# Performance work log

Measured on AMD Instinct MI355X. Metric: run time of the kernel, lower is better.

## Reference

```python
import jax, jax.numpy as jnp
import numpy as np

N_NODES = 100000
N_EDGES = 1000000
D_FEAT = 64


def setup_inputs() -> dict:
    key = jax.random.key(0)
    k1, k2 = jax.random.split(key)
    x = jax.random.normal(k1, (N_NODES, D_FEAT), dtype=jnp.float32)
    es = jax.random.randint(k2, (2, N_EDGES), 0, N_NODES, dtype=jnp.int32)
    return {"x": x, "es": es}


def reference(x, es):
    # message (option='o2i'): col, row = es ; x_i = x[row], x_o = x[col]
    col, row = es[0], es[1]
    x_i = x[row]                              # [E, D]
    x_o = x[col]                              # [E, D]
    msg = jnp.concatenate([x_i, x_o], axis=-1)  # [E, 2D]
    n = x.shape[0]
    # aggregate: scatter-mean over idx=col
    summed = jax.ops.segment_sum(msg, col, num_segments=n)          # [N, 2D]
    ones = jnp.ones((es.shape[1],), dtype=x.dtype)
    count = jax.ops.segment_sum(ones, col, num_segments=n)          # [N]
    count = jnp.maximum(count, 1.0)[:, None]  # clamp(min=1), broadcast
    return summed / count
```

## Files before the change

### kernel.cpp

```cpp
#include <hip/hip_runtime.h>

#define D 64
#define SH 9
#define CPB 512
#define CH 4096
#define MAXNB 256


__global__ __launch_bounds__(256) void count_kernel(
    const int* __restrict__ es, int* __restrict__ cmat,
    int NB, int NBLK, int E) {
  __shared__ int hist[MAXNB];
  int t = threadIdx.x;
  hist[t] = 0;
  __syncthreads();
  int base_e = blockIdx.x * CH;
#pragma unroll
  for (int j = 0; j < 16; j++) {
    int e = base_e + t + j * 256;
    if (e < E) atomicAdd(&hist[es[e] >> SH], 1);
  }
  __syncthreads();
  if (t < NB) cmat[t * NBLK + blockIdx.x] = hist[t];
}

__global__ __launch_bounds__(256) void scanP1(
    int* __restrict__ cmat, int* __restrict__ bsums, int M) {
  __shared__ int lds[256];
  int t = threadIdx.x;
  int base = blockIdx.x * 1024 + t * 4;
  int v[4], s = 0;
#pragma unroll
  for (int i = 0; i < 4; i++) {
    v[i] = (base + i < M) ? cmat[base + i] : 0;
    s += v[i];
  }
  lds[t] = s;
  __syncthreads();
  for (int off = 1; off < 256; off <<= 1) {
    int val = (t >= off) ? lds[t - off] : 0;
    __syncthreads();
    lds[t] += val;
    __syncthreads();
  }
  int run = lds[t] - s;
#pragma unroll
  for (int i = 0; i < 4; i++) {
    if (base + i < M) cmat[base + i] = run;
    run += v[i];
  }
  if (t == 255) bsums[blockIdx.x] = lds[255];
}

__global__ __launch_bounds__(256) void scanP2(
    int* __restrict__ bsums, int* __restrict__ bbase,
    int* __restrict__ offsets, int nb, int NB, int N, int E) {
  __shared__ int lds[256];
  int t = threadIdx.x;
  int v = (t < nb) ? bsums[t] : 0;
  lds[t] = v;
  __syncthreads();
  for (int off = 1; off < 256; off <<= 1) {
    int val = (t >= off) ? lds[t - off] : 0;
    __syncthreads();
    lds[t] += val;
    __syncthreads();
  }
  if (t < nb) bsums[t] = lds[t] - v;
  if (t == 0) { bbase[NB] = E; offsets[N] = E; }
}

__global__ __launch_bounds__(256) void scanP3(
    int* __restrict__ cmat, const int* __restrict__ bsums,
    int* __restrict__ bbase, int M, int NBLK) {
  int t = threadIdx.x;
  int add = bsums[blockIdx.x];
  int base = blockIdx.x * 1024 + t * 4;
#pragma unroll
  for (int i = 0; i < 4; i++) {
    int idx = base + i;
    if (idx < M) {
      int v = cmat[idx] + add;
      cmat[idx] = v;
      if (idx % NBLK == 0) bbase[idx / NBLK] = v;
    }
  }
}

__global__ __launch_bounds__(256) void scatter_kernel(
    const int* __restrict__ es, const int* __restrict__ cmat,
    int* __restrict__ packed, int NB, int NBLK, int E) {
  __shared__ int hist[MAXNB];
  __shared__ int lstart[MAXNB];
  __shared__ int gbase[MAXNB];
  __shared__ int cursor[MAXNB];
  __shared__ int sctmp[256];
  __shared__ int staged[CH];
  __shared__ int bidl[CH];
  int t = threadIdx.x;
  hist[t] = 0;
  __syncthreads();
  int base_e = blockIdx.x * CH;
  int c[16], r[16];
#pragma unroll
  for (int j = 0; j < 16; j++) {
    int e = base_e + t + j * 256;
    if (e < E) {
      c[j] = es[e];
      r[j] = es[E + e];
      atomicAdd(&hist[c[j] >> SH], 1);
    } else {
      c[j] = -1;
    }
  }
  __syncthreads();
  int v = hist[t];
  sctmp[t] = v;
  __syncthreads();
  for (int off = 1; off < 256; off <<= 1) {
    int val = (t >= off) ? sctmp[t - off] : 0;
    __syncthreads();
    sctmp[t] += val;
    __syncthreads();
  }
  int excl = sctmp[t] - v;
  lstart[t] = excl;
  cursor[t] = excl;
  if (t < NB) gbase[t] = cmat[t * NBLK + blockIdx.x];
  __syncthreads();
#pragma unroll
  for (int j = 0; j < 16; j++) {
    if (c[j] >= 0) {
      int b = c[j] >> SH;
      int rank = atomicAdd(&cursor[b], 1);
      staged[rank] = (r[j] << SH) | (c[j] & (CPB - 1));
      bidl[rank] = b;
    }
  }
  __syncthreads();
  int nloc = min(CH, E - base_e);
  for (int i = t; i < nloc; i += 256) {
    int b = bidl[i];
    packed[gbase[b] + (i - lstart[b])] = staged[i];
  }
}

__global__ __launch_bounds__(256) void sort_cols(
    const int* __restrict__ packed, const int* __restrict__ bbase,
    int* __restrict__ offsets, int* __restrict__ sorted_rows, int N) {
  __shared__ int cnt[CPB];
  __shared__ int sctmp[256];
  __shared__ int cur[CPB];
  int b = blockIdx.x;
  int t = threadIdx.x;
  int s = bbase[b], e = bbase[b + 1];
  cnt[t] = 0;
  cnt[t + 256] = 0;
  __syncthreads();
  for (int i = s + t; i < e; i += 256) atomicAdd(&cnt[packed[i] & (CPB - 1)], 1);
  __syncthreads();
  int c0 = cnt[2 * t], c1 = cnt[2 * t + 1];
  int pair = c0 + c1;
  sctmp[t] = pair;
  __syncthreads();
  for (int off = 1; off < 256; off <<= 1) {
    int val = (t >= off) ? sctmp[t - off] : 0;
    __syncthreads();
    sctmp[t] += val;
    __syncthreads();
  }
  int excl = sctmp[t] - pair;
  cur[2 * t] = excl;
  cur[2 * t + 1] = excl + c0;
  int gc0 = (b << SH) + 2 * t;
  if (gc0 < N) offsets[gc0] = s + excl;
  if (gc0 + 1 < N) offsets[gc0 + 1] = s + excl + c0;
  __syncthreads();
  for (int i = s + t; i < e; i += 256) {
    int p = packed[i];
    int cc = p & (CPB - 1);
    int rank = atomicAdd(&cur[cc], 1);
    sorted_rows[s + rank] = p >> SH;
  }
}

__global__ __launch_bounds__(256) void node_reduce(
    const float4* __restrict__ x4, const int* __restrict__ sorted_rows,
    const int* __restrict__ offsets, float* __restrict__ out, int N) {
  int gid = blockIdx.x * 256 + threadIdx.x;
  int node = gid >> 6;
  if (node >= N) return;
  int lane = threadIdx.x & 63;
  int eg = lane >> 4;
  int d16 = lane & 15;
  int start = offsets[node];
  int cnt = offsets[node + 1] - start;
  float4 a0 = make_float4(0.f, 0.f, 0.f, 0.f);
  float4 a1 = make_float4(0.f, 0.f, 0.f, 0.f);
  float4 a2 = make_float4(0.f, 0.f, 0.f, 0.f);
  float4 a3 = make_float4(0.f, 0.f, 0.f, 0.f);
  for (int base = 0; base < cnt; base += 16) {
    int k0 = base + eg;
    int k1 = base + 4 + eg;
    int k2 = base + 8 + eg;
    int k3 = base + 12 + eg;
    int r0 = (k0 < cnt) ? sorted_rows[start + k0] : -1;
    int r1 = (k1 < cnt) ? sorted_rows[start + k1] : -1;
    int r2 = (k2 < cnt) ? sorted_rows[start + k2] : -1;
    int r3 = (k3 < cnt) ? sorted_rows[start + k3] : -1;
    if (r0 >= 0) { float4 v = x4[(size_t)r0 * 16 + d16];
      a0.x += v.x; a0.y += v.y; a0.z += v.z; a0.w += v.w; }
    if (r1 >= 0) { float4 v = x4[(size_t)r1 * 16 + d16];
      a1.x += v.x; a1.y += v.y; a1.z += v.z; a1.w += v.w; }
    if (r2 >= 0) { float4 v = x4[(size_t)r2 * 16 + d16];
      a2.x += v.x; a2.y += v.y; a2.z += v.z; a2.w += v.w; }
    if (r3 >= 0) { float4 v = x4[(size_t)r3 * 16 + d16];
      a3.x += v.x; a3.y += v.y; a3.z += v.z; a3.w += v.w; }
  }
  a0.x += a1.x + a2.x + a3.x;
  a0.y += a1.y + a2.y + a3.y;
  a0.z += a1.z + a2.z + a3.z;
  a0.w += a1.w + a2.w + a3.w;
  a0.x += __shfl_xor(a0.x, 16); a0.y += __shfl_xor(a0.y, 16);
  a0.z += __shfl_xor(a0.z, 16); a0.w += __shfl_xor(a0.w, 16);
  a0.x += __shfl_xor(a0.x, 32); a0.y += __shfl_xor(a0.y, 32);
  a0.z += __shfl_xor(a0.z, 32); a0.w += __shfl_xor(a0.w, 32);
  float4* o4 = (float4*)(out + (size_t)node * 2 * D);
  if (eg == 0) {
    float inv = 1.0f / (float)(cnt > 0 ? cnt : 1);
    a0.x *= inv; a0.y *= inv; a0.z *= inv; a0.w *= inv;
    o4[d16] = a0;
  } else if (eg == 1) {
    float4 v = (cnt > 0) ? x4[(size_t)node * 16 + d16]
                         : make_float4(0.f, 0.f, 0.f, 0.f);
    o4[16 + d16] = v;
  }
}


__global__ __launch_bounds__(256) void edge_scatter_atomic(
    const int* __restrict__ es, const float* __restrict__ x,
    float* __restrict__ out, int* __restrict__ count, int E) {
  int gid = blockIdx.x * blockDim.x + threadIdx.x;
  int e = gid >> 6;
  int lane = gid & 63;
  if (e >= E) return;
  int c = es[e];
  int r = es[E + e];
  if (lane == 0) atomicAdd(&count[c], 1);
  float v = x[(size_t)r * D + lane];
  unsafeAtomicAdd(&out[(size_t)c * 2 * D + lane], v);
}

__global__ __launch_bounds__(256) void finalize_atomic(
    const float* __restrict__ x, float* __restrict__ out,
    const int* __restrict__ count, int N) {
  int gid = blockIdx.x * blockDim.x + threadIdx.x;
  int node = gid >> 5;
  int j4 = gid & 31;
  if (node >= N) return;
  int cnt = count[node];
  float4* out4 = (float4*)(out + (size_t)node * 2 * D);
  if (j4 < 16) {
    float4 s = out4[j4];
    float inv = 1.0f / (float)(cnt > 0 ? cnt : 1);
    s.x *= inv; s.y *= inv; s.z *= inv; s.w *= inv;
    out4[j4] = s;
  } else {
    float4 v;
    if (cnt > 0) {
      const float4* x4 = (const float4*)(x + (size_t)node * D);
      v = x4[j4 - 16];
    } else {
      v = make_float4(0.f, 0.f, 0.f, 0.f);
    }
    out4[j4] = v;
  }
}

extern "C" void kernel_launch(void* const* d_in, const int* in_sizes, int n_in,
                              void* d_out, int out_size, void* d_ws, size_t ws_size,
                              hipStream_t stream) {
  const float* x = (const float*)d_in[0];
  const int* es = (const int*)d_in[1];
  int N = in_sizes[0] / D;
  int E = in_sizes[1] / 2;
  float* out = (float*)d_out;

  int NB = (N + CPB - 1) >> SH;
  int NBLK = (E + CH - 1) / CH;
  int M = NB * NBLK;
  int nb2 = (M + 1023) / 1024;
  size_t need = ((size_t)M + 256 + (NB + 1) + ((size_t)N + 1) +
                 2 * (size_t)E) * sizeof(int);
  if (NB > MAXNB || nb2 > 256 || ws_size < need) {
    int* count = (int*)d_ws;
    hipMemsetAsync(count, 0, (size_t)N * sizeof(int), stream);
    hipMemsetAsync(out, 0, (size_t)N * 2 * D * sizeof(float), stream);
    long long t1 = (long long)E * 64;
    edge_scatter_atomic<<<(int)((t1 + 255) / 256), 256, 0, stream>>>(es, x, out, count, E);
    long long t2 = (long long)N * 32;
    finalize_atomic<<<(int)((t2 + 255) / 256), 256, 0, stream>>>(x, out, count, N);
    return;
  }

  int* ws = (int*)d_ws;
  int* cmat = ws;
  int* bsums = cmat + M;
  int* bbase = bsums + 256;
  int* offsets = bbase + NB + 1;
  int* packed = offsets + N + 1;
  int* sorted_rows = packed + E;

  count_kernel<<<NBLK, 256, 0, stream>>>(es, cmat, NB, NBLK, E);
  scanP1<<<nb2, 256, 0, stream>>>(cmat, bsums, M);
  scanP2<<<1, 256, 0, stream>>>(bsums, bbase, offsets, nb2, NB, N, E);
  scanP3<<<nb2, 256, 0, stream>>>(cmat, bsums, bbase, M, NBLK);
  scatter_kernel<<<NBLK, 256, 0, stream>>>(es, cmat, packed, NB, NBLK, E);
  sort_cols<<<NB, 256, 0, stream>>>(packed, bbase, offsets, sorted_rows, N);

  long long rt = (long long)N * 64;
  node_reduce<<<(int)((rt + 255) / 256), 256, 0, stream>>>(
      (const float4*)x, sorted_rows, offsets, out, N);
}
```

Before: 162.2 us.

## Replace two-level bucket sort with atomic-count CSR build via global atomics

```diff
diff --git a/kernel.cpp b/kernel.cpp
--- a/kernel.cpp
+++ b/kernel.cpp
@@ -1,38 +1,34 @@
 #include <hip/hip_runtime.h>
 
 #define D 64
-#define SH 9
-#define CPB 512
-#define CH 4096
-#define MAXNB 256
-
-
-__global__ __launch_bounds__(256) void count_kernel(
-    const int* __restrict__ es, int* __restrict__ cmat,
-    int NB, int NBLK, int E) {
-  __shared__ int hist[MAXNB];
-  int t = threadIdx.x;
-  hist[t] = 0;
-  __syncthreads();
-  int base_e = blockIdx.x * CH;
-#pragma unroll
-  for (int j = 0; j < 16; j++) {
-    int e = base_e + t + j * 256;
-    if (e < E) atomicAdd(&hist[es[e] >> SH], 1);
-  }
-  __syncthreads();
-  if (t < NB) cmat[t * NBLK + blockIdx.x] = hist[t];
+
+
+__global__ __launch_bounds__(256) void deg_count(
+    const int* __restrict__ es, int* __restrict__ count, int E) {
+  int t = blockIdx.x * 256 + threadIdx.x;
+  int base = t * 8;
+  if (base + 8 <= E) {
+    const int4* p = (const int4*)(es + base);
+    int4 a = p[0], b = p[1];
+    atomicAdd(&count[a.x], 1); atomicAdd(&count[a.y], 1);
+    atomicAdd(&count[a.z], 1); atomicAdd(&count[a.w], 1);
+    atomicAdd(&count[b.x], 1); atomicAdd(&count[b.y], 1);
+    atomicAdd(&count[b.z], 1); atomicAdd(&count[b.w], 1);
+  } else {
+    for (int e = base; e < E; e++) atomicAdd(&count[es[e]], 1);
+  }
 }
 
 __global__ __launch_bounds__(256) void scanP1(
-    int* __restrict__ cmat, int* __restrict__ bsums, int M) {
+    const int* __restrict__ count, int* __restrict__ offsets,
+    int* __restrict__ bsums, int N) {
   __shared__ int lds[256];
   int t = threadIdx.x;
   int base = blockIdx.x * 1024 + t * 4;
   int v[4], s = 0;
 #pragma unroll
   for (int i = 0; i < 4; i++) {
-    v[i] = (base + i < M) ? cmat[base + i] : 0;
+    v[i] = (base + i < N) ? count[base + i] : 0;
     s += v[i];
   }
   lds[t] = s;
@@ -46,15 +42,14 @@
   int run = lds[t] - s;
 #pragma unroll
   for (int i = 0; i < 4; i++) {
-    if (base + i < M) cmat[base + i] = run;
+    if (base + i < N) offsets[base + i] = run;
     run += v[i];
   }
   if (t == 255) bsums[blockIdx.x] = lds[255];
 }
 
 __global__ __launch_bounds__(256) void scanP2(
-    int* __restrict__ bsums, int* __restrict__ bbase,
-    int* __restrict__ offsets, int nb, int NB, int N, int E) {
+    int* __restrict__ bsums, int nb) {
   __shared__ int lds[256];
   int t = threadIdx.x;
   int v = (t < nb) ? bsums[t] : 0;
@@ -67,134 +62,59 @@
     __syncthreads();
   }
   if (t < nb) bsums[t] = lds[t] - v;
-  if (t == 0) { bbase[NB] = E; offsets[N] = E; }
 }
 
 __global__ __launch_bounds__(256) void scanP3(
-    int* __restrict__ cmat, const int* __restrict__ bsums,
-    int* __restrict__ bbase, int M, int NBLK) {
+    int* __restrict__ offsets, const int* __restrict__ bsums, int N) {
   int t = threadIdx.x;
   int add = bsums[blockIdx.x];
   int base = blockIdx.x * 1024 + t * 4;
 #pragma unroll
   for (int i = 0; i < 4; i++) {
     int idx = base + i;
-    if (idx < M) {
-      int v = cmat[idx] + add;
-      cmat[idx] = v;
-      if (idx % NBLK == 0) bbase[idx / NBLK] = v;
+    if (idx < N) offsets[idx] += add;
+  }
+}
+
+__global__ __launch_bounds__(256) void place(
+    const int* __restrict__ es, int* __restrict__ offsets,
+    int* __restrict__ sorted_rows, int E) {
+  int t = blockIdx.x * 256 + threadIdx.x;
+  int base = t * 8;
+  if (base + 8 <= E) {
+    const int4* pc = (const int4*)(es + base);
+    const int4* pr = (const int4*)(es + E + base);
+    int4 c0 = pc[0], c1 = pc[1];
+    int4 r0 = pr[0], r1 = pr[1];
+    int p;
+    p = atomicAdd(&offsets[c0.x], 1); sorted_rows[p] = r0.x;
+    p = atomicAdd(&offsets[c0.y], 1); sorted_rows[p] = r0.y;
+    p = atomicAdd(&offsets[c0.z], 1); sorted_rows[p] = r0.z;
+    p = atomicAdd(&offsets[c0.w], 1); sorted_rows[p] = r0.w;
+    p = atomicAdd(&offsets[c1.x], 1); sorted_rows[p] = r1.x;
+    p = atomicAdd(&offsets[c1.y], 1); sorted_rows[p] = r1.y;
+    p = atomicAdd(&offsets[c1.z], 1); sorted_rows[p] = r1.z;
+    p = atomicAdd(&offsets[c1.w], 1); sorted_rows[p] = r1.w;
+  } else {
+    for (int e = base; e < E; e++) {
+      int p = atomicAdd(&offsets[es[e]], 1);
+      sorted_rows[p] = es[E + e];
     }
-  }
-}
-
-__global__ __launch_bounds__(256) void scatter_kernel(
-    const int* __restrict__ es, const int* __restrict__ cmat,
-    int* __restrict__ packed, int NB, int NBLK, int E) {
-  __shared__ int hist[MAXNB];
-  __shared__ int lstart[MAXNB];
-  __shared__ int gbase[MAXNB];
-  __shared__ int cursor[MAXNB];
-  __shared__ int sctmp[256];
-  __shared__ int staged[CH];
-  __shared__ int bidl[CH];
-  int t = threadIdx.x;
-  hist[t] = 0;
-  __syncthreads();
-  int base_e = blockIdx.x * CH;
-  int c[16], r[16];
-#pragma unroll
-  for (int j = 0; j < 16; j++) {
-    int e = base_e + t + j * 256;
-    if (e < E) {
-      c[j] = es[e];
-      r[j] = es[E + e];
-      atomicAdd(&hist[c[j] >> SH], 1);
-    } else {
-      c[j] = -1;
-    }
-  }
-  __syncthreads();
-  int v = hist[t];
-  sctmp[t] = v;
-  __syncthreads();
-  for (int off = 1; off < 256; off <<= 1) {
-    int val = (t >= off) ? sctmp[t - off] : 0;
-    __syncthreads();
-    sctmp[t] += val;
-    __syncthreads();
-  }
-  int excl = sctmp[t] - v;
-  lstart[t] = excl;
-  cursor[t] = excl;
-  if (t < NB) gbase[t] = cmat[t * NBLK + blockIdx.x];
-  __syncthreads();
-#pragma unroll
-  for (int j = 0; j < 16; j++) {
-    if (c[j] >= 0) {
-      int b = c[j] >> SH;
-      int rank = atomicAdd(&cursor[b], 1);
-      staged[rank] = (r[j] << SH) | (c[j] & (CPB - 1));
-      bidl[rank] = b;
-    }
-  }
-  __syncthreads();
-  int nloc = min(CH, E - base_e);
-  for (int i = t; i < nloc; i += 256) {
-    int b = bidl[i];
-    packed[gbase[b] + (i - lstart[b])] = staged[i];
-  }
-}
-
-__global__ __launch_bounds__(256) void sort_cols(
-    const int* __restrict__ packed, const int* __restrict__ bbase,
-    int* __restrict__ offsets, int* __restrict__ sorted_rows, int N) {
-  __shared__ int cnt[CPB];
-  __shared__ int sctmp[256];
-  __shared__ int cur[CPB];
-  int b = blockIdx.x;
-  int t = threadIdx.x;
-  int s = bbase[b], e = bbase[b + 1];
-  cnt[t] = 0;
-  cnt[t + 256] = 0;
-  __syncthreads();
-  for (int i = s + t; i < e; i += 256) atomicAdd(&cnt[packed[i] & (CPB - 1)], 1);
-  __syncthreads();
-  int c0 = cnt[2 * t], c1 = cnt[2 * t + 1];
-  int pair = c0 + c1;
-  sctmp[t] = pair;
-  __syncthreads();
-  for (int off = 1; off < 256; off <<= 1) {
-    int val = (t >= off) ? sctmp[t - off] : 0;
-    __syncthreads();
-    sctmp[t] += val;
-    __syncthreads();
-  }
-  int excl = sctmp[t] - pair;
-  cur[2 * t] = excl;
-  cur[2 * t + 1] = excl + c0;
-  int gc0 = (b << SH) + 2 * t;
-  if (gc0 < N) offsets[gc0] = s + excl;
-  if (gc0 + 1 < N) offsets[gc0 + 1] = s + excl + c0;
-  __syncthreads();
-  for (int i = s + t; i < e; i += 256) {
-    int p = packed[i];
-    int cc = p & (CPB - 1);
-    int rank = atomicAdd(&cur[cc], 1);
-    sorted_rows[s + rank] = p >> SH;
   }
 }
 
 __global__ __launch_bounds__(256) void node_reduce(
     const float4* __restrict__ x4, const int* __restrict__ sorted_rows,
-    const int* __restrict__ offsets, float* __restrict__ out, int N) {
+    const int* __restrict__ offsets, const int* __restrict__ count,
+    float* __restrict__ out, int N) {
   int gid = blockIdx.x * 256 + threadIdx.x;
   int node = gid >> 6;
   if (node >= N) return;
   int lane = threadIdx.x & 63;
   int eg = lane >> 4;
   int d16 = lane & 15;
-  int start = offsets[node];
-  int cnt = offsets[node + 1] - start;
+  int cnt = count[node];
+  int start = offsets[node] - cnt;
   float4 a0 = make_float4(0.f, 0.f, 0.f, 0.f);
   float4 a1 = make_float4(0.f, 0.f, 0.f, 0.f);
   float4 a2 = make_float4(0.f, 0.f, 0.f, 0.f);
@@ -287,13 +207,9 @@
   int E = in_sizes[1] / 2;
   float* out = (float*)d_out;
 
-  int NB = (N + CPB - 1) >> SH;
-  int NBLK = (E + CH - 1) / CH;
-  int M = NB * NBLK;
-  int nb2 = (M + 1023) / 1024;
-  size_t need = ((size_t)M + 256 + (NB + 1) + ((size_t)N + 1) +
-                 2 * (size_t)E) * sizeof(int);
-  if (NB > MAXNB || nb2 > 256 || ws_size < need) {
+  int nb1 = (N + 1023) / 1024;
+  size_t need = ((size_t)N + ((size_t)N + 1) + (size_t)E + 256) * sizeof(int);
+  if (nb1 > 256 || ws_size < need) {
     int* count = (int*)d_ws;
     hipMemsetAsync(count, 0, (size_t)N * sizeof(int), stream);
     hipMemsetAsync(out, 0, (size_t)N * 2 * D * sizeof(float), stream);
@@ -305,21 +221,21 @@
   }
 
   int* ws = (int*)d_ws;
-  int* cmat = ws;
-  int* bsums = cmat + M;
-  int* bbase = bsums + 256;
-  int* offsets = bbase + NB + 1;
-  int* packed = offsets + N + 1;
-  int* sorted_rows = packed + E;
-
-  count_kernel<<<NBLK, 256, 0, stream>>>(es, cmat, NB, NBLK, E);
-  scanP1<<<nb2, 256, 0, stream>>>(cmat, bsums, M);
-  scanP2<<<1, 256, 0, stream>>>(bsums, bbase, offsets, nb2, NB, N, E);
-  scanP3<<<nb2, 256, 0, stream>>>(cmat, bsums, bbase, M, NBLK);
-  scatter_kernel<<<NBLK, 256, 0, stream>>>(es, cmat, packed, NB, NBLK, E);
-  sort_cols<<<NB, 256, 0, stream>>>(packed, bbase, offsets, sorted_rows, N);
+  int* count = ws;
+  int* offsets = count + N;
+  int* sorted_rows = offsets + N + 1;
+  int* bsums = sorted_rows + E;
+
+  hipMemsetAsync(count, 0, (size_t)N * sizeof(int), stream);
+
+  int eblk = (E + 2047) / 2048;
+  deg_count<<<eblk, 256, 0, stream>>>(es, count, E);
+  scanP1<<<nb1, 256, 0, stream>>>(count, offsets, bsums, N);
+  scanP2<<<1, 256, 0, stream>>>(bsums, nb1);
+  scanP3<<<nb1, 256, 0, stream>>>(offsets, bsums, N);
+  place<<<eblk, 256, 0, stream>>>(es, offsets, sorted_rows, E);
 
   long long rt = (long long)N * 64;
   node_reduce<<<(int)((rt + 255) / 256), 256, 0, stream>>>(
-      (const float4*)x, sorted_rows, offsets, out, N);
-}
+      (const float4*)x, sorted_rows, offsets, count, out, N);
+}
```

Result: slower. 247.0 us (+52.3%).
